# Kernel tuning notes

Hardware: AMD Instinct MI355X
Metric: run time of the kernel (lower is better)

Reference implementation:

```python
import jax, jax.numpy as jnp
import numpy as np

B, S, D, H = 4, 2048, 1024, 16
DH = D // H  # attention_head_size = 64


def setup_inputs() -> dict:
    key = jax.random.key(0)
    ks = jax.random.split(key, 9)
    scale = 1.0 / np.sqrt(D)
    x = jax.random.normal(ks[0], (B, S, D), dtype=jnp.float32)
    Wq = jax.random.normal(ks[1], (H, D, DH), dtype=jnp.float32) * scale
    Wk = jax.random.normal(ks[2], (H, D, DH), dtype=jnp.float32) * scale
    Wv = jax.random.normal(ks[3], (H, D, DH), dtype=jnp.float32) * scale
    bq = jax.random.normal(ks[4], (H, DH), dtype=jnp.float32) * 0.01
    bk = jax.random.normal(ks[5], (H, DH), dtype=jnp.float32) * 0.01
    bv = jax.random.normal(ks[6], (H, DH), dtype=jnp.float32) * 0.01
    Wo = jax.random.normal(ks[7], (D, D), dtype=jnp.float32) * scale
    bo = jax.random.normal(ks[8], (D,), dtype=jnp.float32) * 0.01
    return {"x": x, "Wq": Wq, "bq": bq, "Wk": Wk, "bk": bk,
            "Wv": Wv, "bv": bv, "Wo": Wo, "bo": bo}


def reference(x, Wq, bq, Wk, bk, Wv, bv, Wo, bo):
    # Per-head Linear projections, stacked over the head axis h.
    q = jnp.einsum('bsd,hde->bhse', x, Wq) + bq[None, :, None, :]
    k = jnp.einsum('bsd,hde->bhse', x, Wk) + bk[None, :, None, :]
    v = jnp.einsum('bsd,hde->bhse', x, Wv) + bv[None, :, None, :]
    # QK^T / sqrt(dh), softmax over keys (axis=-1), then @ V.
    scores = jnp.einsum('bhse,bhte->bhst', q, k) / jnp.sqrt(jnp.float32(DH))
    attn = jax.nn.softmax(scores, axis=-1)
    ctx = jnp.einsum('bhst,bhte->bhse', attn, v)
    # Concatenate heads along the feature axis: [B,S,H*DH].
    concat = jnp.transpose(ctx, (0, 2, 1, 3)).reshape(B, S, H * DH)
    # Output projection (dropout is identity in inference).
    return concat @ Wo + bo
```

## Files before the change

### kernel.cpp

```cpp
#include <hip/hip_runtime.h>


#define Bn  4
#define Sn  2048
#define Dn  1024
#define Hn  16
#define DHn 64
#define Mn  (Bn*Sn)
#define LDKV 72

typedef unsigned short u16;
typedef __attribute__((ext_vector_type(8))) short short8;
typedef __attribute__((ext_vector_type(4))) float f32x4;
typedef __attribute__((ext_vector_type(2))) unsigned int uint2v;
typedef __attribute__((ext_vector_type(4))) unsigned int uint4v;

__device__ __forceinline__ u16 f2bf(float f) {
  unsigned u = __float_as_uint(f);
  return (u16)((u + 0x7FFFu + ((u >> 16) & 1u)) >> 16);
}

__device__ __forceinline__ void async16(const void* g, void* l) {
  __builtin_amdgcn_global_load_lds(
      (const __attribute__((address_space(1))) void*)g,
      (__attribute__((address_space(3))) void*)l, 16, 0, 0);
}

__device__ __forceinline__ unsigned pk2(float a, float b) {
  return __builtin_amdgcn_perm(__float_as_uint(b), __float_as_uint(a), 0x07060302u);
}

__global__ __launch_bounds__(256) void k_convert(
    const float4* __restrict__ x, ushort4* __restrict__ xb, int n4,
    const float* __restrict__ Wq, const float* __restrict__ Wk,
    const float* __restrict__ Wv, const float* __restrict__ Wo,
    u16* __restrict__ WqT, u16* __restrict__ WkT,
    u16* __restrict__ WvT, u16* __restrict__ WoT) {
  __shared__ float t[64][65];
  const int bid0 = blockIdx.x;
  if (bid0 < 8192) {
    int i = bid0 * 256 + threadIdx.x;
    if (i < n4) {
      float4 f = x[i];
      ushort4 o;
      o.x = f2bf(f.x); o.y = f2bf(f.y); o.z = f2bf(f.z); o.w = f2bf(f.w);
      xb[i] = o;
    }
    return;
  }
  const int bid = bid0 - 8192;
  const int wsel = bid >> 8;
  const int idx = bid & 255;
  const int tid = threadIdx.x;
  const int c = tid & 63;
  const int r4 = tid >> 6;

  if (wsel < 3) {
    const float* W = (wsel == 0) ? Wq : (wsel == 1) ? Wk : Wv;
    u16* T = (wsel == 0) ? WqT : (wsel == 1) ? WkT : WvT;
    const int h = idx >> 4;
    const int d0 = (idx & 15) * 64;
    const float* src = W + (size_t)h * (Dn * DHn) + (size_t)d0 * DHn;
#pragma unroll
    for (int r = 0; r < 16; r++) {
      int row = r * 4 + r4;
      t[row][c] = src[row * DHn + c];
    }
    __syncthreads();
    u16* dst = T + (size_t)(h * 64) * Dn + d0;
#pragma unroll
    for (int r = 0; r < 16; r++) {
      int erow = r * 4 + r4;
      dst[(size_t)erow * Dn + c] = f2bf(t[c][erow]);
    }
  } else {
    const int n0 = (idx >> 4) * 64;
    const int d0 = (idx & 15) * 64;
#pragma unroll
    for (int r = 0; r < 16; r++) {
      int row = r * 4 + r4;
      t[row][c] = Wo[(size_t)(d0 + row) * Dn + n0 + c];
    }
    __syncthreads();
#pragma unroll
    for (int r = 0; r < 16; r++) {
      int nrow = r * 4 + r4;
      WoT[(size_t)(n0 + nrow) * Dn + d0 + c] = f2bf(t[c][nrow]);
    }
  }
}

template<int SWAP>
__device__ __forceinline__ void qkv_body(
    u16* As, u16* Bs, const u16* __restrict__ A, const u16* __restrict__ BT,
    const float* __restrict__ bias, u16* __restrict__ dst, float scale,
    int tile_m, int tile_n) {
  const int K = Dn;
  const int tid = threadIdx.x;
  const int lane = tid & 63;
  const int wave = tid >> 6;
  const int wm = wave & 3, wn = wave >> 2;
  const int quad = lane >> 4, l16 = lane & 15;
  const int srow8 = lane >> 3;
  const int gchunk = (lane & 7) ^ srow8;
  const int sw = l16 & 7;

  f32x4 acc[2][4];
#pragma unroll
  for (int i = 0; i < 2; i++)
#pragma unroll
    for (int j = 0; j < 4; j++) acc[i][j] = (f32x4){0.f, 0.f, 0.f, 0.f};

  for (int k0 = 0; k0 < K; k0 += 64) {
    const int rb = wave * 16;
    async16(&A[(size_t)(tile_m + rb + srow8) * K + k0 + gchunk * 8], &As[rb * 64]);
    async16(&A[(size_t)(tile_m + rb + 8 + srow8) * K + k0 + gchunk * 8], &As[(rb + 8) * 64]);
    async16(&BT[(size_t)(tile_n + rb + srow8) * K + k0 + gchunk * 8], &Bs[rb * 64]);
    async16(&BT[(size_t)(tile_n + rb + 8 + srow8) * K + k0 + gchunk * 8], &Bs[(rb + 8) * 64]);
    __syncthreads();
#pragma unroll
    for (int ks = 0; ks < 2; ++ks) {
      short8 a[2], b[4];
#pragma unroll
      for (int i = 0; i < 2; i++)
        a[i] = *(const short8*)&As[(wm * 32 + i * 16 + l16) * 64 + ((ks * 4 + quad) ^ sw) * 8];
#pragma unroll
      for (int j = 0; j < 4; j++)
        b[j] = *(const short8*)&Bs[(wn * 64 + j * 16 + l16) * 64 + ((ks * 4 + quad) ^ sw) * 8];
#pragma unroll
      for (int i = 0; i < 2; i++)
#pragma unroll
        for (int j = 0; j < 4; j++)
          acc[i][j] = SWAP
              ? __builtin_amdgcn_mfma_f32_16x16x32_bf16(b[j], a[i], acc[i][j], 0, 0, 0)
              : __builtin_amdgcn_mfma_f32_16x16x32_bf16(a[i], b[j], acc[i][j], 0, 0, 0);
    }
    __syncthreads();
  }

  if (SWAP) {
#pragma unroll
    for (int i = 0; i < 2; i++) {
      const int s = tile_m + wm * 32 + i * 16 + l16;
      const int bb = s >> 11, sl = s & 2047;
#pragma unroll
      for (int j = 0; j < 4; j++) {
        const int nb = tile_n + wn * 64 + j * 16 + quad * 4;
        const float4 b4 = *(const float4*)&bias[nb];
        const int h = nb >> 6, e0 = nb & 63;
        ushort4 o;
        o.x = f2bf((acc[i][j][0] + b4.x) * scale);
        o.y = f2bf((acc[i][j][1] + b4.y) * scale);
        o.z = f2bf((acc[i][j][2] + b4.z) * scale);
        o.w = f2bf((acc[i][j][3] + b4.w) * scale);
        *(ushort4*)&dst[((size_t)(bb * Hn + h) * Sn + sl) * DHn + e0] = o;
      }
    }
  } else {
#pragma unroll
    for (int i = 0; i < 2; i++) {
      const int s0 = tile_m + wm * 32 + i * 16 + quad * 4;
      const int bb = s0 >> 11, sl = s0 & 2047;
#pragma unroll
      for (int j = 0; j < 4; j++) {
        const int n = tile_n + wn * 64 + j * 16 + l16;
        const int h = n >> 6, e = n & 63;
        const float bn = bias[n];
        ushort4 o;
        o.x = f2bf(acc[i][j][0] + bn);
        o.y = f2bf(acc[i][j][1] + bn);
        o.z = f2bf(acc[i][j][2] + bn);
        o.w = f2bf(acc[i][j][3] + bn);
        *(ushort4*)&dst[((size_t)(bb * Hn + h) * DHn + e) * Sn + sl] = o;
      }
    }
  }
}

__global__ __launch_bounds__(512) void k_gemm_qkv(
    const u16* __restrict__ A, const u16* __restrict__ WqT,
    const u16* __restrict__ WkT, const u16* __restrict__ WvT,
    const float* __restrict__ bq, const float* __restrict__ bk,
    const float* __restrict__ bv, u16* __restrict__ qb,
    u16* __restrict__ kb, u16* __restrict__ vtb) {
  __shared__ u16 As[128 * 64];
  __shared__ u16 Bs[128 * 64];
  const int p = blockIdx.x;
  const int i = p >> 3;
  const int mt = (p & 7) * 8 + (i & 7);
  const int zn = i >> 3;
  const int z = zn >> 3;
  const int tile_m = mt * 128;
  const int tile_n = (zn & 7) * 128;
  if (z == 2) {
    qkv_body<0>(As, Bs, A, WvT, bv, vtb, 1.0f, tile_m, tile_n);
  } else if (z == 1) {
    qkv_body<1>(As, Bs, A, WkT, bk, kb, 1.0f, tile_m, tile_n);
  } else {
    qkv_body<1>(As, Bs, A, WqT, bq, qb, 0.18033688011112042f, tile_m, tile_n);
  }
}

__global__ __launch_bounds__(256) void k_attn(
    const u16* __restrict__ qg, const u16* __restrict__ kg,
    const u16* __restrict__ vg, u16* __restrict__ ctx) {
  const int p = blockIdx.x;
  const int logical = (p & 7) * 128 + (p >> 3);
  const int bh = logical >> 4;
  const int b = bh >> 4, h = bh & 15;
  const int tid = threadIdx.x;
  const int wave = tid >> 6, lane = tid & 63;
  const int quad = lane >> 4, l16 = lane & 15;
  const int qbase = (logical & 15) * 128 + wave * 32;

  const u16* qp = qg + (size_t)bh * Sn * DHn;
  const u16* kp = kg + (size_t)bh * Sn * DHn;
  const u16* vp = vg + (size_t)bh * DHn * Sn;

  __shared__ u16 Ks[2][64 * 64];
  __shared__ u16 Vs[2][64 * LDKV];

  const int srow8 = lane >> 3;
  const int gchunk = (lane & 7) ^ srow8;
  const int sw = l16 & 7;

  const int vrow = tid >> 3;
  const int vc = tid & 7;

  const int r0 = wave * 16 + srow8;
  const int r1 = r0 + 8;
  const int pk0 = ((r0 >> 5) << 5) | (((r0 >> 2) & 3) << 3) | ((r0 & 16) >> 2) | (r0 & 3);
  const int pk1 = ((r1 >> 5) << 5) | (((r1 >> 2) & 3) << 3) | ((r1 & 16) >> 2) | (r1 & 3);

  short8 bq[2][2];
#pragma unroll
  for (int g2 = 0; g2 < 2; g2++) {
    bq[g2][0] = *(const short8*)&qp[(size_t)(qbase + g2 * 16 + l16) * DHn + quad * 8];
    bq[g2][1] = *(const short8*)&qp[(size_t)(qbase + g2 * 16 + l16) * DHn + 32 + quad * 8];
  }

  f32x4 octx[2][4];
#pragma unroll
  for (int g2 = 0; g2 < 2; g2++)
#pragma unroll
    for (int j = 0; j < 4; j++) octx[g2][j] = (f32x4){0.f, 0.f, 0.f, 0.f};
  f32x4 octl[2];
  octl[0] = (f32x4){0.f, 0.f, 0.f, 0.f};
  octl[1] = (f32x4){0.f, 0.f, 0.f, 0.f};
  const short8 vones = {(short)0x3F80, (short)0x3F80, (short)0x3F80, (short)0x3F80,
                        (short)0x3F80, (short)0x3F80, (short)0x3F80, (short)0x3F80};

  {
    const int rbase = wave * 16;
    async16(&kp[(size_t)pk0 * DHn + gchunk * 8], &Ks[0][rbase * 64]);
    async16(&kp[(size_t)pk1 * DHn + gchunk * 8], &Ks[0][(rbase + 8) * 64]);
    uint4 vv0 = *(const uint4*)&vp[(size_t)vrow * Sn + vc * 8];
    uint4 vv1 = *(const uint4*)&vp[(size_t)(32 + vrow) * Sn + vc * 8];
    *(uint4*)&Vs[0][vrow * LDKV + vc * 8] = vv0;
    *(uint4*)&Vs[0][(32 + vrow) * LDKV + vc * 8] = vv1;
  }
  __syncthreads();

  uint4 vv0, vv1;
  for (int kt = 0; kt < Sn / 64; ++kt) {
    const int cur = kt & 1, nxt = cur ^ 1;
    const bool more = (kt + 1 < Sn / 64);
    if (more) {
      const int key1 = (kt + 1) * 64;
      const int rbase = wave * 16;
      async16(&kp[(size_t)(key1 + pk0) * DHn + gchunk * 8], &Ks[nxt][rbase * 64]);
      async16(&kp[(size_t)(key1 + pk1) * DHn + gchunk * 8], &Ks[nxt][(rbase + 8) * 64]);
      vv0 = *(const uint4*)&vp[(size_t)vrow * Sn + key1 + vc * 8];
      vv1 = *(const uint4*)&vp[(size_t)(32 + vrow) * Sn + key1 + vc * 8];
    }

    uint4v apv[2][2];
#pragma unroll
    for (int g = 0; g < 4; g++) {
      short8 ka0 = *(const short8*)&Ks[cur][(g * 16 + l16) * 64 + (quad ^ sw) * 8];
      short8 ka1 = *(const short8*)&Ks[cur][(g * 16 + l16) * 64 + ((quad + 4) ^ sw) * 8];
#pragma unroll
      for (int g2 = 0; g2 < 2; g2++) {
        f32x4 sc = (f32x4){0.f, 0.f, 0.f, 0.f};
        sc = __builtin_amdgcn_mfma_f32_16x16x32_bf16(ka0, bq[g2][0], sc, 0, 0, 0);
        sc = __builtin_amdgcn_mfma_f32_16x16x32_bf16(ka1, bq[g2][1], sc, 0, 0, 0);
        float p4[4];
#pragma unroll
        for (int r = 0; r < 4; r++) p4[r] = __builtin_amdgcn_exp2f(sc[r]);
        apv[g2][g >> 1][(g & 1) * 2]     = pk2(p4[0], p4[1]);
        apv[g2][g >> 1][(g & 1) * 2 + 1] = pk2(p4[2], p4[3]);
      }
    }

#pragma unroll
    for (int P = 0; P < 2; P++) {
      octl[0] = __builtin_amdgcn_mfma_f32_16x16x32_bf16(
          __builtin_bit_cast(short8, apv[0][P]), vones, octl[0], 0, 0, 0);
      octl[1] = __builtin_amdgcn_mfma_f32_16x16x32_bf16(
          __builtin_bit_cast(short8, apv[1][P]), vones, octl[1], 0, 0, 0);
    }
#pragma unroll
    for (int j = 0; j < 4; j++) {
#pragma unroll
      for (int P = 0; P < 2; P++) {
        short8 vb = *(const short8*)&Vs[cur][(j * 16 + l16) * LDKV + P * 32 + quad * 8];
        octx[0][j] = __builtin_amdgcn_mfma_f32_16x16x32_bf16(
            __builtin_bit_cast(short8, apv[0][P]), vb, octx[0][j], 0, 0, 0);
        octx[1][j] = __builtin_amdgcn_mfma_f32_16x16x32_bf16(
            __builtin_bit_cast(short8, apv[1][P]), vb, octx[1][j], 0, 0, 0);
      }
    }

    if (more) {
      *(uint4*)&Vs[nxt][vrow * LDKV + vc * 8] = vv0;
      *(uint4*)&Vs[nxt][(32 + vrow) * LDKV + vc * 8] = vv1;
    }
    __syncthreads();
  }

  float rl[2][4];
#pragma unroll
  for (int g2 = 0; g2 < 2; g2++)
#pragma unroll
    for (int r = 0; r < 4; r++)
      rl[g2][r] = 1.0f / octl[g2][r];

#pragma unroll
  for (int g2 = 0; g2 < 2; g2++)
#pragma unroll
    for (int j = 0; j < 4; j++) {
      const int n = h * DHn + j * 16 + l16;
#pragma unroll
      for (int r = 0; r < 4; r++) {
        const int s = qbase + g2 * 16 + quad * 4 + r;
        ctx[(size_t)(b * Sn + s) * Dn + n] = f2bf(octx[g2][j][r] * rl[g2][r]);
      }
    }
}

__global__ __launch_bounds__(512) void k_gemm_out(
    const u16* __restrict__ A, const u16* __restrict__ WoT,
    const float* __restrict__ bo, float* __restrict__ out) {
  const int p = blockIdx.x;
  const int i0 = p >> 3;
  const int tile_m = ((p & 7) * 8 + (i0 & 7)) * 128;
  const int tile_n = (i0 >> 3) * 128;
  const int K = Dn;

  __shared__ u16 As[128 * 64];
  __shared__ u16 Bs[128 * 64];

  const int tid = threadIdx.x;
  const int lane = tid & 63;
  const int wave = tid >> 6;
  const int wm = wave & 3, wn = wave >> 2;
  const int quad = lane >> 4, l16 = lane & 15;
  const int srow8 = lane >> 3;
  const int gchunk = (lane & 7) ^ srow8;
  const int sw = l16 & 7;

  f32x4 acc[2][4];
#pragma unroll
  for (int i = 0; i < 2; i++)
#pragma unroll
    for (int j = 0; j < 4; j++) acc[i][j] = (f32x4){0.f, 0.f, 0.f, 0.f};

  for (int k0 = 0; k0 < K; k0 += 64) {
    const int rb = wave * 16;
    async16(&A[(size_t)(tile_m + rb + srow8) * K + k0 + gchunk * 8], &As[rb * 64]);
    async16(&A[(size_t)(tile_m + rb + 8 + srow8) * K + k0 + gchunk * 8], &As[(rb + 8) * 64]);
    async16(&WoT[(size_t)(tile_n + rb + srow8) * K + k0 + gchunk * 8], &Bs[rb * 64]);
    async16(&WoT[(size_t)(tile_n + rb + 8 + srow8) * K + k0 + gchunk * 8], &Bs[(rb + 8) * 64]);
    __syncthreads();
#pragma unroll
    for (int ks = 0; ks < 2; ++ks) {
      short8 a[2], b[4];
#pragma unroll
      for (int i = 0; i < 2; i++)
        a[i] = *(const short8*)&As[(wm * 32 + i * 16 + l16) * 64 + ((ks * 4 + quad) ^ sw) * 8];
#pragma unroll
      for (int j = 0; j < 4; j++)
        b[j] = *(const short8*)&Bs[(wn * 64 + j * 16 + l16) * 64 + ((ks * 4 + quad) ^ sw) * 8];
#pragma unroll
      for (int i = 0; i < 2; i++)
#pragma unroll
        for (int j = 0; j < 4; j++)
          acc[i][j] = __builtin_amdgcn_mfma_f32_16x16x32_bf16(b[j], a[i], acc[i][j], 0, 0, 0);
    }
    __syncthreads();
  }

#pragma unroll
  for (int i = 0; i < 2; i++) {
    const int s = tile_m + wm * 32 + i * 16 + l16;
#pragma unroll
    for (int j = 0; j < 4; j++) {
      const int nb = tile_n + wn * 64 + j * 16 + quad * 4;
      const float4 b4 = *(const float4*)&bo[nb];
      float4 o;
      o.x = acc[i][j][0] + b4.x;
      o.y = acc[i][j][1] + b4.y;
      o.z = acc[i][j][2] + b4.z;
      o.w = acc[i][j][3] + b4.w;
      *(float4*)&out[(size_t)s * Dn + nb] = o;
    }
  }
}

extern "C" void kernel_launch(void* const* d_in, const int* in_sizes, int n_in,
                              void* d_out, int out_size, void* d_ws, size_t ws_size,
                              hipStream_t stream) {
  const float* x  = (const float*)d_in[0];
  const float* Wq = (const float*)d_in[1];
  const float* bq = (const float*)d_in[2];
  const float* Wk = (const float*)d_in[3];
  const float* bk = (const float*)d_in[4];
  const float* Wv = (const float*)d_in[5];
  const float* bv = (const float*)d_in[6];
  const float* Wo = (const float*)d_in[7];
  const float* bo = (const float*)d_in[8];
  float* out = (float*)d_out;

  char* ws = (char*)d_ws;
  u16* xb  = (u16*)ws;  ws += (size_t)Mn * Dn * 2;
  u16* WqT = (u16*)ws;  ws += (size_t)Dn * Dn * 2;
  u16* WkT = (u16*)ws;  ws += (size_t)Dn * Dn * 2;
  u16* WvT = (u16*)ws;  ws += (size_t)Dn * Dn * 2;
  u16* WoT = (u16*)ws;  ws += (size_t)Dn * Dn * 2;
  u16* qb  = (u16*)ws;  ws += (size_t)Mn * Dn * 2;
  u16* kb  = (u16*)ws;  ws += (size_t)Mn * Dn * 2;
  u16* vtb = (u16*)ws;  ws += (size_t)Mn * Dn * 2;
  u16* ctx = xb;

  k_convert<<<8192 + 1024, 256, 0, stream>>>(
      (const float4*)x, (ushort4*)xb, Mn * Dn / 4,
      Wq, Wk, Wv, Wo, WqT, WkT, WvT, WoT);

  k_gemm_qkv<<<(Mn / 128) * (Dn / 128) * 3, 512, 0, stream>>>(
      xb, WqT, WkT, WvT, bq, bk, bv, qb, kb, vtb);

  k_attn<<<(Sn / 128) * Bn * Hn, 256, 0, stream>>>(qb, kb, vtb, ctx);

  k_gemm_out<<<(Mn / 128) * (Dn / 128), 512, 0, stream>>>(ctx, WoT, bo, out);
}
```

Baseline: 266.2 us.

## Software-pipeline attention: overlap QK^T/exp of tile k with PV of tile k-1

Restructures the attention inner loop so each iteration computes the scores and exponentials for the current key tile while issuing the P·V and row-sum MFMAs for the previous tile's probabilities, interleaved per 16-row group. A prologue handles the first tile and an epilogue finishes the last PV. The aim is to hide exp/pack latency behind matrix-core work. In exchange the loop now needs an extra __syncthreads per iteration and holds more live registers for the previous tile's probabilities.

```diff
diff --git a/kernel.cpp b/kernel.cpp
--- a/kernel.cpp
+++ b/kernel.cpp
@@ -223,11 +223,12 @@
   const int srow8 = lane >> 3;
   const int gchunk = (lane & 7) ^ srow8;
   const int sw = l16 & 7;
+  const int rbase = wave * 16;
 
   const int vrow = tid >> 3;
   const int vc = tid & 7;
 
-  const int r0 = wave * 16 + srow8;
+  const int r0 = rbase + srow8;
   const int r1 = r0 + 8;
   const int pk0 = ((r0 >> 5) << 5) | (((r0 >> 2) & 3) << 3) | ((r0 & 16) >> 2) | (r0 & 3);
   const int pk1 = ((r1 >> 5) << 5) | (((r1 >> 2) & 3) << 3) | ((r1 & 16) >> 2) | (r1 & 3);
@@ -251,34 +252,27 @@
                         (short)0x3F80, (short)0x3F80, (short)0x3F80, (short)0x3F80};
 
   {
-    const int rbase = wave * 16;
     async16(&kp[(size_t)pk0 * DHn + gchunk * 8], &Ks[0][rbase * 64]);
     async16(&kp[(size_t)pk1 * DHn + gchunk * 8], &Ks[0][(rbase + 8) * 64]);
-    uint4 vv0 = *(const uint4*)&vp[(size_t)vrow * Sn + vc * 8];
-    uint4 vv1 = *(const uint4*)&vp[(size_t)(32 + vrow) * Sn + vc * 8];
-    *(uint4*)&Vs[0][vrow * LDKV + vc * 8] = vv0;
-    *(uint4*)&Vs[0][(32 + vrow) * LDKV + vc * 8] = vv1;
+    uint4 v0 = *(const uint4*)&vp[(size_t)vrow * Sn + vc * 8];
+    uint4 v1 = *(const uint4*)&vp[(size_t)(32 + vrow) * Sn + vc * 8];
+    *(uint4*)&Vs[0][vrow * LDKV + vc * 8] = v0;
+    *(uint4*)&Vs[0][(32 + vrow) * LDKV + vc * 8] = v1;
   }
   __syncthreads();
 
+  uint4v apv_prev[2][2];
   uint4 vv0, vv1;
-  for (int kt = 0; kt < Sn / 64; ++kt) {
-    const int cur = kt & 1, nxt = cur ^ 1;
-    const bool more = (kt + 1 < Sn / 64);
-    if (more) {
-      const int key1 = (kt + 1) * 64;
-      const int rbase = wave * 16;
-      async16(&kp[(size_t)(key1 + pk0) * DHn + gchunk * 8], &Ks[nxt][rbase * 64]);
-      async16(&kp[(size_t)(key1 + pk1) * DHn + gchunk * 8], &Ks[nxt][(rbase + 8) * 64]);
-      vv0 = *(const uint4*)&vp[(size_t)vrow * Sn + key1 + vc * 8];
-      vv1 = *(const uint4*)&vp[(size_t)(32 + vrow) * Sn + key1 + vc * 8];
-    }
-
-    uint4v apv[2][2];
+
+  {
+    async16(&kp[(size_t)(64 + pk0) * DHn + gchunk * 8], &Ks[1][rbase * 64]);
+    async16(&kp[(size_t)(64 + pk1) * DHn + gchunk * 8], &Ks[1][(rbase + 8) * 64]);
+    vv0 = *(const uint4*)&vp[(size_t)vrow * Sn + 64 + vc * 8];
+    vv1 = *(const uint4*)&vp[(size_t)(32 + vrow) * Sn + 64 + vc * 8];
 #pragma unroll
     for (int g = 0; g < 4; g++) {
-      short8 ka0 = *(const short8*)&Ks[cur][(g * 16 + l16) * 64 + (quad ^ sw) * 8];
-      short8 ka1 = *(const short8*)&Ks[cur][(g * 16 + l16) * 64 + ((quad + 4) ^ sw) * 8];
+      short8 ka0 = *(const short8*)&Ks[0][(g * 16 + l16) * 64 + (quad ^ sw) * 8];
+      short8 ka1 = *(const short8*)&Ks[0][(g * 16 + l16) * 64 + ((quad + 4) ^ sw) * 8];
 #pragma unroll
       for (int g2 = 0; g2 < 2; g2++) {
         f32x4 sc = (f32x4){0.f, 0.f, 0.f, 0.f};
@@ -287,35 +281,98 @@
         float p4[4];
 #pragma unroll
         for (int r = 0; r < 4; r++) p4[r] = __builtin_amdgcn_exp2f(sc[r]);
+        apv_prev[g2][g >> 1][(g & 1) * 2]     = pk2(p4[0], p4[1]);
+        apv_prev[g2][g >> 1][(g & 1) * 2 + 1] = pk2(p4[2], p4[3]);
+      }
+    }
+    *(uint4*)&Vs[1][vrow * LDKV + vc * 8] = vv0;
+    *(uint4*)&Vs[1][(32 + vrow) * LDKV + vc * 8] = vv1;
+    __syncthreads();
+  }
+
+  for (int kt = 1; kt < Sn / 64; ++kt) {
+    const int cur = kt & 1, nxt = cur ^ 1;
+    const bool more = (kt + 1 < Sn / 64);
+    if (more) {
+      const int key1 = (kt + 1) * 64;
+      async16(&kp[(size_t)(key1 + pk0) * DHn + gchunk * 8], &Ks[nxt][rbase * 64]);
+      async16(&kp[(size_t)(key1 + pk1) * DHn + gchunk * 8], &Ks[nxt][(rbase + 8) * 64]);
+      vv0 = *(const uint4*)&vp[(size_t)vrow * Sn + key1 + vc * 8];
+      vv1 = *(const uint4*)&vp[(size_t)(32 + vrow) * Sn + key1 + vc * 8];
+    }
+
+    uint4v apv[2][2];
+#pragma unroll
+    for (int g = 0; g < 4; g++) {
+      short8 ka0 = *(const short8*)&Ks[cur][(g * 16 + l16) * 64 + (quad ^ sw) * 8];
+      short8 ka1 = *(const short8*)&Ks[cur][(g * 16 + l16) * 64 + ((quad + 4) ^ sw) * 8];
+#pragma unroll
+      for (int g2 = 0; g2 < 2; g2++) {
+        f32x4 sc = (f32x4){0.f, 0.f, 0.f, 0.f};
+        sc = __builtin_amdgcn_mfma_f32_16x16x32_bf16(ka0, bq[g2][0], sc, 0, 0, 0);
+        sc = __builtin_amdgcn_mfma_f32_16x16x32_bf16(ka1, bq[g2][1], sc, 0, 0, 0);
+        float p4[4];
+#pragma unroll
+        for (int r = 0; r < 4; r++) p4[r] = __builtin_amdgcn_exp2f(sc[r]);
         apv[g2][g >> 1][(g & 1) * 2]     = pk2(p4[0], p4[1]);
         apv[g2][g >> 1][(g & 1) * 2 + 1] = pk2(p4[2], p4[3]);
       }
-    }
-
-#pragma unroll
-    for (int P = 0; P < 2; P++) {
-      octl[0] = __builtin_amdgcn_mfma_f32_16x16x32_bf16(
-          __builtin_bit_cast(short8, apv[0][P]), vones, octl[0], 0, 0, 0);
-      octl[1] = __builtin_amdgcn_mfma_f32_16x16x32_bf16(
-          __builtin_bit_cast(short8, apv[1][P]), vones, octl[1], 0, 0, 0);
-    }
-#pragma unroll
-    for (int j = 0; j < 4; j++) {
-#pragma unroll
-      for (int P = 0; P < 2; P++) {
-        short8 vb = *(const short8*)&Vs[cur][(j * 16 + l16) * LDKV + P * 32 + quad * 8];
-        octx[0][j] = __builtin_amdgcn_mfma_f32_16x16x32_bf16(
-            __builtin_bit_cast(short8, apv[0][P]), vb, octx[0][j], 0, 0, 0);
-        octx[1][j] = __builtin_amdgcn_mfma_f32_16x16x32_bf16(
-            __builtin_bit_cast(short8, apv[1][P]), vb, octx[1][j], 0, 0, 0);
-      }
-    }
-
+      short8 vb0 = *(const short8*)&Vs[nxt][(g * 16 + l16) * LDKV + quad * 8];
+      short8 vb1 = *(const short8*)&Vs[nxt][(g * 16 + l16) * LDKV + 32 + quad * 8];
+      octx[0][g] = __builtin_amdgcn_mfma_f32_16x16x32_bf16(
+          __builtin_bit_cast(short8, apv_prev[0][0]), vb0, octx[0][g], 0, 0, 0);
+      octx[1][g] = __builtin_amdgcn_mfma_f32_16x16x32_bf16(
+          __builtin_bit_cast(short8, apv_prev[1][0]), vb0, octx[1][g], 0, 0, 0);
+      octx[0][g] = __builtin_amdgcn_mfma_f32_16x16x32_bf16(
+          __builtin_bit_cast(short8, apv_prev[0][1]), vb1, octx[0][g], 0, 0, 0);
+      octx[1][g] = __builtin_amdgcn_mfma_f32_16x16x32_bf16(
+          __builtin_bit_cast(short8, apv_prev[1][1]), vb1, octx[1][g], 0, 0, 0);
+      if (g == 0) {
+        octl[0] = __builtin_amdgcn_mfma_f32_16x16x32_bf16(
+            __builtin_bit_cast(short8, apv_prev[0][0]), vones, octl[0], 0, 0, 0);
+        octl[1] = __builtin_amdgcn_mfma_f32_16x16x32_bf16(
+            __builtin_bit_cast(short8, apv_prev[1][0]), vones, octl[1], 0, 0, 0);
+      }
+      if (g == 1) {
+        octl[0] = __builtin_amdgcn_mfma_f32_16x16x32_bf16(
+            __builtin_bit_cast(short8, apv_prev[0][1]), vones, octl[0], 0, 0, 0);
+        octl[1] = __builtin_amdgcn_mfma_f32_16x16x32_bf16(
+            __builtin_bit_cast(short8, apv_prev[1][1]), vones, octl[1], 0, 0, 0);
+      }
+    }
+
+    __syncthreads();
     if (more) {
       *(uint4*)&Vs[nxt][vrow * LDKV + vc * 8] = vv0;
       *(uint4*)&Vs[nxt][(32 + vrow) * LDKV + vc * 8] = vv1;
     }
     __syncthreads();
+
+#pragma unroll
+    for (int g2 = 0; g2 < 2; g2++)
+#pragma unroll
+      for (int P = 0; P < 2; P++) apv_prev[g2][P] = apv[g2][P];
+  }
+
+#pragma unroll
+  for (int g = 0; g < 4; g++) {
+    short8 vb0 = *(const short8*)&Vs[1][(g * 16 + l16) * LDKV + quad * 8];
+    short8 vb1 = *(const short8*)&Vs[1][(g * 16 + l16) * LDKV + 32 + quad * 8];
+    octx[0][g] = __builtin_amdgcn_mfma_f32_16x16x32_bf16(
+        __builtin_bit_cast(short8, apv_prev[0][0]), vb0, octx[0][g], 0, 0, 0);
+    octx[1][g] = __builtin_amdgcn_mfma_f32_16x16x32_bf16(
+        __builtin_bit_cast(short8, apv_prev[1][0]), vb0, octx[1][g], 0, 0, 0);
+    octx[0][g] = __builtin_amdgcn_mfma_f32_16x16x32_bf16(
+        __builtin_bit_cast(short8, apv_prev[0][1]), vb1, octx[0][g], 0, 0, 0);
+    octx[1][g] = __builtin_amdgcn_mfma_f32_16x16x32_bf16(
+        __builtin_bit_cast(short8, apv_prev[1][1]), vb1, octx[1][g], 0, 0, 0);
+  }
+#pragma unroll
+  for (int P = 0; P < 2; P++) {
+    octl[0] = __builtin_amdgcn_mfma_f32_16x16x32_bf16(
+        __builtin_bit_cast(short8, apv_prev[0][P]), vones, octl[0], 0, 0, 0);
+    octl[1] = __builtin_amdgcn_mfma_f32_16x16x32_bf16(
+        __builtin_bit_cast(short8, apv_prev[1][P]), vones, octl[1], 0, 0, 0);
   }
 
   float rl[2][4];
```

New measurement: 292.5 us. +9.9%, slower.
